# Performance work log

Measured on AMD Instinct MI355X. Metric: run time of the kernel, lower is better.

The kernel has to match this reference:

```python
import jax, jax.numpy as jnp
import numpy as np

D = 1024
H = 16
HD = D // H
DFF = 4 * D
LN_EPS = 1e-5

def layernorm(x, gamma, beta):
    mu = jnp.mean(x, axis=-1, keepdims=True)
    var = jnp.mean(jnp.square(x - mu), axis=-1, keepdims=True)
    return (x - mu) * jax.lax.rsqrt(var + LN_EPS) * gamma + beta

def setup_inputs() -> dict:
    key = jax.random.key(0)
    ks = jax.random.split(key, 10)
    B, Nq, Nk = 2, 2048, 2048
    s = 0.02
    return {
        "q_x": jax.random.normal(ks[0], (B, Nq, D), jnp.float32),
        "kv_x": jax.random.normal(ks[1], (B, Nk, D), jnp.float32),
        "Wq": jax.random.normal(ks[2], (D, D), jnp.float32) * s,
        "Wkv": jax.random.normal(ks[3], (2 * D, D), jnp.float32) * s,
        "Wo": jax.random.normal(ks[4], (D, D), jnp.float32) * s,
        "bo": jnp.zeros((D,), jnp.float32),
        "ln_q_g": jnp.ones((D,), jnp.float32),
        "ln_q_b": jnp.zeros((D,), jnp.float32),
        "ln_kv_g": jnp.ones((D,), jnp.float32),
        "ln_kv_b": jnp.zeros((D,), jnp.float32),
        "W1": jax.random.normal(ks[5], (DFF, D), jnp.float32) * s,
        "b1": jnp.zeros((DFF,), jnp.float32),
        "W2": jax.random.normal(ks[6], (D, DFF), jnp.float32) * s,
        "b2": jnp.zeros((D,), jnp.float32),
    }

def reference(q_x, kv_x, Wq, Wkv, Wo, bo, ln_q_g, ln_q_b, ln_kv_g, ln_kv_b, W1, b1, W2, b2):
    B, Nq, _ = q_x.shape
    Nk = kv_x.shape[1]
    scale = HD ** -0.5
    # norm + projections
    q = layernorm(q_x, ln_q_g, ln_q_b) @ Wq.T                    # [B,Nq,D]
    kv = layernorm(kv_x, ln_kv_g, ln_kv_b) @ Wkv.T               # [B,Nk,2D]
    q = q.reshape(B, Nq, H, HD).transpose(0, 2, 1, 3)            # [B,H,Nq,hd]
    kv = kv.reshape(B, Nk, 2, H, HD).transpose(2, 0, 3, 1, 4)    # [2,B,H,Nk,hd]
    k, v = kv[0], kv[1]
    attn = jnp.einsum('bhqd,bhkd->bhqk', q, k) * scale           # [B,H,Nq,Nk]
    attn = jax.nn.softmax(attn, axis=-1)
    out = jnp.einsum('bhqk,bhkd->bhqd', attn, v)
    out = out.transpose(0, 2, 1, 3).reshape(B, Nq, D)
    x = q_x + out @ Wo.T + bo
    h = jax.nn.silu(x @ W1.T + b1)
    x = x + h @ W2.T + b2
    return x
```

## Files before the change

### kernel.cpp

```cpp
#include <hip/hip_runtime.h>

using u16   = unsigned short;
using f32x4 = __attribute__((ext_vector_type(4))) float;
using s16x8 = __attribute__((ext_vector_type(8))) short;
using u32x2 = __attribute__((ext_vector_type(2))) unsigned int;
using u32x4 = __attribute__((ext_vector_type(4))) unsigned int;

#define LOG2E 1.44269504088896f

static __device__ __forceinline__ u16 f2bf(float f) {
  union { float f; unsigned u; } a; a.f = f;
  unsigned r = a.u + 0x7fffu + ((a.u >> 16) & 1u);
  return (u16)(r >> 16);
}
static __device__ __forceinline__ unsigned cvtpk(float lo, float hi) {
  unsigned r;
  asm("v_cvt_pk_bf16_f32 %0, %1, %2" : "=v"(r) : "v"(lo), "v"(hi));
  return r;
}

static __device__ __forceinline__ void gload16(const void* g, void* l) {
  __builtin_amdgcn_global_load_lds(
      (__attribute__((address_space(1))) unsigned int*)g,
      (__attribute__((address_space(3))) unsigned int*)l, 16, 0, 0);
}

static __device__ __forceinline__ int xcd_swz(int b, int nb) {
  return (b & 7) * (nb >> 3) + (b >> 3);
}

__global__ __launch_bounds__(256) void prep_k(
    const float* __restrict__ Wq, const float* __restrict__ Wkv,
    const float* __restrict__ Wo, const float* __restrict__ W1,
    const float* __restrict__ W2,
    u16* __restrict__ wq_b, u16* __restrict__ wkv_b, u16* __restrict__ wo_b,
    u16* __restrict__ w1_b, u16* __restrict__ w2_b,
    const float* __restrict__ xq, const float* __restrict__ xk,
    const float* __restrict__ gq, const float* __restrict__ bq,
    const float* __restrict__ gk, const float* __restrict__ bk,
    u16* __restrict__ oq, u16* __restrict__ ok)
{
  const int blk = blockIdx.x, t = threadIdx.x;
  if (blk < 12288) {
    const int i = blk * 256 + t;
    const float* src; u16* dst; int off; float sc = 1.0f;
    if      (i <  262144) { src = Wq;  dst = wq_b;  off = i; sc = 0.125f * LOG2E; }
    else if (i <  786432) { src = Wkv; dst = wkv_b; off = i -  262144; }
    else if (i < 1048576) { src = Wo;  dst = wo_b;  off = i -  786432; }
    else if (i < 2097152) { src = W1;  dst = w1_b;  off = i - 1048576; }
    else                  { src = W2;  dst = w2_b;  off = i - 2097152; }
    const float4 v = ((const float4*)src)[off];
    ushort4 o;
    o.x = f2bf(v.x * sc); o.y = f2bf(v.y * sc); o.z = f2bf(v.z * sc); o.w = f2bf(v.w * sc);
    ((ushort4*)dst)[off] = o;
    return;
  }
  int row = blk - 12288;
  const float* x; const float* gam; const float* bet; u16* out;
  if (row < 4096) { x = xq; gam = gq; bet = bq; out = oq; }
  else { row -= 4096; x = xk; gam = gk; bet = bk; out = ok; }
  const float4 v = ((const float4*)(x + (size_t)row * 1024))[t];
  float s  = v.x + v.y + v.z + v.w;
  float ss = v.x*v.x + v.y*v.y + v.z*v.z + v.w*v.w;
  #pragma unroll
  for (int m = 1; m < 64; m <<= 1) { s += __shfl_xor(s, m); ss += __shfl_xor(ss, m); }
  __shared__ float red[8];
  const int w = t >> 6;
  if ((t & 63) == 0) { red[w] = s; red[4 + w] = ss; }
  __syncthreads();
  s  = red[0] + red[1] + red[2] + red[3];
  ss = red[4] + red[5] + red[6] + red[7];
  const float mu   = s * (1.0f / 1024.0f);
  const float rstd = rsqrtf(ss * (1.0f / 1024.0f) - mu * mu + 1e-5f);
  const float4 gv = ((const float4*)gam)[t];
  const float4 bv = ((const float4*)bet)[t];
  ushort4 o;
  o.x = f2bf((v.x - mu) * rstd * gv.x + bv.x);
  o.y = f2bf((v.y - mu) * rstd * gv.y + bv.y);
  o.z = f2bf((v.z - mu) * rstd * gv.z + bv.z);
  o.w = f2bf((v.w - mu) * rstd * gv.w + bv.w);
  ((ushort4*)(out + (size_t)row * 1024))[t] = o;
}

template<int BIAS, int RES, int SILU, int OF32, int OBF>
static __device__ __forceinline__ void gemm_body64(
    const u16* __restrict__ A, const u16* __restrict__ B,
    u16* __restrict__ Cb, float* __restrict__ Cf,
    const float* __restrict__ bias, const float* __restrict__ resid,
    int N, int K, int bid, u16* smem)
{
  const int tid = threadIdx.x;
  const int w = tid >> 6, l = tid & 63;
  const int g = l >> 4, q = l & 15;
  const int ntn = N >> 6;
  const int bm = bid / ntn, bn = bid - bm * ntn;
  const int wr = w >> 1, wc = w & 1;
  const int sw = (q & 7) << 4;
  f32x4 acc[2][2] = {};

  const size_t abase = (size_t)(bm * 128) * K;
  const size_t bbase = (size_t)(bn * 64) * K;

  auto stage = [&](int buf, int k0) {
    u16* as = smem + buf * 8192;
    u16* bs = smem + 16384 + buf * 4096;
    #pragma unroll
    for (int r = 0; r < 2; ++r) {
      const int c = (r << 9) + tid;
      const int row = c >> 3;
      const int sp = (c & 7) ^ (row & 7);
      gload16(A + abase + (size_t)row * K + k0 + sp * 8,
              as + (size_t)((r << 9) + (w << 6)) * 8);
    }
    const int row = tid >> 3;
    const int sp = (tid & 7) ^ (row & 7);
    gload16(B + bbase + (size_t)row * K + k0 + sp * 8,
            bs + (size_t)(w << 6) * 8);
  };

  const int NT = K >> 6;
  stage(0, 0);
  asm volatile("s_waitcnt vmcnt(0)" ::: "memory");
  __syncthreads();
  int cur = 0;
  for (int t = 0; t < NT; ++t) {
    if (t + 1 < NT) stage(cur ^ 1, (t + 1) << 6);
    const char* as = (const char*)(smem + cur * 8192);
    const char* bs = (const char*)(smem + 16384 + cur * 4096);
    #pragma unroll
    for (int ks = 0; ks < 2; ++ks) {
      s16x8 af[2], bfr[2];
      #pragma unroll
      for (int m = 0; m < 2; ++m)
        af[m] = *(const s16x8*)(as + (size_t)(wr * 32 + m * 16 + q) * 128 +
                                ((ks * 64 + g * 16) ^ sw));
      #pragma unroll
      for (int n = 0; n < 2; ++n)
        bfr[n] = *(const s16x8*)(bs + (size_t)(wc * 32 + n * 16 + q) * 128 +
                                 ((ks * 64 + g * 16) ^ sw));
      #pragma unroll
      for (int m = 0; m < 2; ++m)
        #pragma unroll
        for (int n = 0; n < 2; ++n)
          acc[m][n] = __builtin_amdgcn_mfma_f32_16x16x32_bf16(af[m], bfr[n], acc[m][n], 0, 0, 0);
    }
    asm volatile("s_waitcnt vmcnt(0)" ::: "memory");
    __syncthreads();
    cur ^= 1;
  }

  #pragma unroll
  for (int m = 0; m < 2; ++m) {
    const int row0 = bm * 128 + wr * 32 + m * 16 + g * 4;
    #pragma unroll
    for (int n = 0; n < 2; ++n) {
      const int col = bn * 64 + wc * 32 + n * 16 + q;
      float bv = 0.0f;
      if (BIAS) bv = bias[col];
      #pragma unroll
      for (int r = 0; r < 4; ++r) {
        const size_t idx = (size_t)(row0 + r) * N + col;
        float v = acc[m][n][r] + bv;
        if (RES)  v += resid[idx];
        if (SILU) v = v / (1.0f + __expf(-v));
        if (OF32) Cf[idx] = v;
        if (OBF)  Cb[idx] = f2bf(v);
      }
    }
  }
}

template<int BIAS, int RES, int SILU, int OF32, int OBF>
__global__ __launch_bounds__(512, 4) void gemm_k(
    const u16* __restrict__ A, const u16* __restrict__ B,
    u16* __restrict__ Cb, float* __restrict__ Cf,
    const float* __restrict__ bias, const float* __restrict__ resid,
    int N, int K)
{
  __shared__ u16 smem[24576];
  const int bid = xcd_swz(blockIdx.x, gridDim.x);
  gemm_body64<BIAS, RES, SILU, OF32, OBF>(A, B, Cb, Cf, bias, resid, N, K, bid, smem);
}

__global__ __launch_bounds__(512, 4) void gemm_qkv_k(
    const u16* __restrict__ lnq, const u16* __restrict__ wq, u16* __restrict__ qp,
    const u16* __restrict__ lnk, const u16* __restrict__ wkv, u16* __restrict__ kvp)
{
  __shared__ u16 smem[24576];
  const int sbid = xcd_swz(blockIdx.x, 1536);
  if (sbid < 512)
    gemm_body64<0,0,0,0,1>(lnq, wq, qp, nullptr, nullptr, nullptr, 1024, 1024,
                           sbid, smem);
  else
    gemm_body64<0,0,0,0,1>(lnk, wkv, kvp, nullptr, nullptr, nullptr, 2048, 1024,
                           sbid - 512, smem);
}

template<int BIAS, int RES, int SILU, int OF32, int OBF>
__global__ __launch_bounds__(512, 2) void gemm256_k(
    const u16* __restrict__ A, const u16* __restrict__ B,
    u16* __restrict__ Cb, float* __restrict__ Cf,
    const float* __restrict__ bias, const float* __restrict__ resid,
    int N, int K)
{
  __shared__ u16 smem[65536];
  char* smem_c = (char*)smem;
  const int tid = threadIdx.x;
  const int w = tid >> 6, l = tid & 63;
  const int g = l >> 4, q = l & 15;
  const int wm = w >> 2, wn = w & 3;
  const int ntn = N >> 8;
  const int bid = xcd_swz(blockIdx.x, gridDim.x);
  const int bm = bid / ntn, bn = bid - bm * ntn;

  const size_t abase = (size_t)(bm * 256) * K;
  const size_t bbase = (size_t)(bn * 256) * K;

  f32x4 acc[8][4] = {};

  auto stage2 = [&](int buf, int kt, int part) {
    const int isB = part & 1, khalf = part >> 1;
    #pragma unroll
    for (int sub = 0; sub < 2; ++sub) {
      const int row  = sub * 128 + (tid >> 2);
      const int slot = (tid & 3) ^ ((row >> 1) & 3);
      const u16* src = (isB ? B + bbase : A + abase)
                     + (size_t)row * K + kt * 64 + khalf * 32 + slot * 8;
      char* dst = smem_c + buf * 65536 + isB * 32768 + khalf * 16384
                + sub * 8192 + w * 1024;
      gload16(src, dst);
    }
  };

  const int NT = K >> 6;
  stage2(0, 0, 0); stage2(0, 0, 1); stage2(0, 0, 2); stage2(0, 0, 3);
  int cur = 0;
  const int so = (g ^ ((q >> 1) & 3)) * 16;
  for (int t = 0; t < NT; ++t) {
    const bool pre = (t + 1 < NT);
    const char* base = smem_c + cur * 65536;
    #pragma unroll
    for (int ks = 0; ks < 2; ++ks) {
      if (ks == 0 || pre) asm volatile("s_waitcnt vmcnt(4)" ::: "memory");
      else                asm volatile("s_waitcnt vmcnt(0)" ::: "memory");
      asm volatile("" ::: "memory");
      __builtin_amdgcn_s_barrier();
      asm volatile("" ::: "memory");
      const char* Ab = base + ks * 16384;
      const char* Bb = base + 32768 + ks * 16384;
      s16x8 af[8], bf0[2];
      #pragma unroll
      for (int m = 0; m < 8; ++m)
        af[m] = *(const s16x8*)(Ab + (wm * 128 + m * 16 + q) * 64 + so);
      #pragma unroll
      for (int n = 0; n < 2; ++n)
        bf0[n] = *(const s16x8*)(Bb + (wn * 64 + n * 16 + q) * 64 + so);
      if (pre) stage2(cur ^ 1, t + 1, ks * 2);
      asm volatile("s_waitcnt lgkmcnt(0)" ::: "memory");
      __builtin_amdgcn_sched_barrier(0);
      __builtin_amdgcn_s_setprio(1);
      #pragma unroll
      for (int m = 0; m < 8; ++m) {
        acc[m][0] = __builtin_amdgcn_mfma_f32_16x16x32_bf16(af[m], bf0[0], acc[m][0], 0, 0, 0);
        acc[m][1] = __builtin_amdgcn_mfma_f32_16x16x32_bf16(af[m], bf0[1], acc[m][1], 0, 0, 0);
      }
      __builtin_amdgcn_s_setprio(0);
      s16x8 bf1[2];
      #pragma unroll
      for (int n = 0; n < 2; ++n)
        bf1[n] = *(const s16x8*)(Bb + (wn * 64 + (2 + n) * 16 + q) * 64 + so);
      if (pre) stage2(cur ^ 1, t + 1, ks * 2 + 1);
      asm volatile("s_waitcnt lgkmcnt(0)" ::: "memory");
      __builtin_amdgcn_sched_barrier(0);
      __builtin_amdgcn_s_setprio(1);
      #pragma unroll
      for (int m = 0; m < 8; ++m) {
        acc[m][2] = __builtin_amdgcn_mfma_f32_16x16x32_bf16(af[m], bf1[0], acc[m][2], 0, 0, 0);
        acc[m][3] = __builtin_amdgcn_mfma_f32_16x16x32_bf16(af[m], bf1[1], acc[m][3], 0, 0, 0);
      }
      __builtin_amdgcn_s_setprio(0);
    }
    cur ^= 1;
  }

  #pragma unroll
  for (int m = 0; m < 8; ++m) {
    const int row0 = bm * 256 + wm * 128 + m * 16 + g * 4;
    #pragma unroll
    for (int n = 0; n < 4; ++n) {
      const int col = bn * 256 + wn * 64 + n * 16 + q;
      float bv = 0.0f;
      if (BIAS) bv = bias[col];
      #pragma unroll
      for (int r = 0; r < 4; ++r) {
        const size_t idx = (size_t)(row0 + r) * N + col;
        float v = acc[m][n][r] + bv;
        if (RES)  v += resid[idx];
        if (SILU) v = v / (1.0f + __expf(-v));
        if (OF32) Cf[idx] = v;
        if (OBF)  Cb[idx] = f2bf(v);
      }
    }
  }
}

__global__ __launch_bounds__(256, 4) void attn_k(
    const u16* __restrict__ Q, const u16* __restrict__ KV, u16* __restrict__ O)
{
  __shared__ u16 Ks[2][64 * 64];
  __shared__ u16 Vs[2][64 * 64];
  const int tid = threadIdx.x;
  const int w = tid >> 6, l = tid & 63;
  const int g = l >> 4, q = l & 15;
  const int idx = blockIdx.x >> 3;
  const int bh = (blockIdx.x & 7) * 4 + (idx >> 5);
  const int qt = idx & 31;
  const int b = bh >> 4, h = bh & 15;

  const size_t qrow = (size_t)(b * 2048 + qt * 64 + w * 16 + q);
  s16x8 qf[2];
  qf[0] = *(const s16x8*)&Q[qrow * 1024 + h * 64 + g * 8];
  qf[1] = *(const s16x8*)&Q[qrow * 1024 + h * 64 + 32 + g * 8];

  f32x4 oacc[4] = {};
  float lrow = 0.0f;

  const u16* kvb = KV + (size_t)b * 2048 * 2048;
  const unsigned vs_base =
      (unsigned)(unsigned long long)(__attribute__((address_space(3))) u16*)Vs;

  auto stage = [&](int buf, int kv0) {
    #pragma unroll
    for (int r = 0; r < 2; ++r) {
      const int c = (r << 8) + tid;
      const int krow = c >> 3, slot = c & 7;
      gload16(kvb + (size_t)(kv0 + krow) * 2048 + h * 64 + ((slot ^ (krow & 7)) << 3),
              &Ks[buf][(size_t)((r << 8) + (w << 6)) * 8]);
      const int vkv = ((c >> 3) & 15) * 4 + ((c >> 1) & 3);
      const int vd0 = ((c >> 7) & 3) * 16 + (c & 1) * 8;
      gload16(kvb + (size_t)(kv0 + vkv) * 2048 + 1024 + h * 64 + vd0,
              &Vs[buf][(size_t)((r << 8) + (w << 6)) * 8]);
    }
  };

  stage(0, 0);
  asm volatile("s_waitcnt vmcnt(0)" ::: "memory");
  __syncthreads();
  int cur = 0;

  for (int kt = 0; kt < 32; ++kt) {
    if (kt + 1 < 32) stage(cur ^ 1, (kt + 1) * 64);

    const char* ksb = (const char*)Ks[cur];
    f32x4 sacc[4] = {};
    __builtin_amdgcn_s_setprio(1);
    #pragma unroll
    for (int s = 0; s < 2; ++s)
      #pragma unroll
      for (int nf = 0; nf < 4; ++nf) {
        const int krw = nf * 16 + q;
        const s16x8 kf = *(const s16x8*)(ksb + krw * 128 +
                              ((s * 64 + g * 16) ^ ((krw & 7) << 4)));
        sacc[nf] = __builtin_amdgcn_mfma_f32_16x16x32_bf16(kf, qf[s], sacc[nf], 0, 0, 0);
      }
    __builtin_amdgcn_s_setprio(0);

    #pragma unroll
    for (int nf = 0; nf < 4; ++nf)
      #pragma unroll
      for (int r = 0; r < 4; ++r)
        sacc[nf][r] = __builtin_amdgcn_exp2f(sacc[nf][r]);
    float rs0 = (sacc[0][0] + sacc[0][1]) + (sacc[0][2] + sacc[0][3]);
    float rs1 = (sacc[1][0] + sacc[1][1]) + (sacc[1][2] + sacc[1][3]);
    float rs2 = (sacc[2][0] + sacc[2][1]) + (sacc[2][2] + sacc[2][3]);
    float rs3 = (sacc[3][0] + sacc[3][1]) + (sacc[3][2] + sacc[3][3]);
    float rs = (rs0 + rs1) + (rs2 + rs3);
    rs += __shfl_xor(rs, 16);
    rs += __shfl_xor(rs, 32);
    lrow += rs;

    union { u32x4 u; s16x8 s8; } au[2];
    #pragma unroll
    for (int s = 0; s < 2; ++s) {
      au[s].u[0] = cvtpk(sacc[2*s  ][0], sacc[2*s  ][1]);
      au[s].u[1] = cvtpk(sacc[2*s  ][2], sacc[2*s  ][3]);
      au[s].u[2] = cvtpk(sacc[2*s+1][0], sacc[2*s+1][1]);
      au[s].u[3] = cvtpk(sacc[2*s+1][2], sacc[2*s+1][3]);
    }

    const unsigned a0 = vs_base + (unsigned)(cur << 13) + (unsigned)(g * 128 + 2 * q);
    u32x2 v0,v1,v2,v3,v4,v5,v6,v7,v8,v9,v10,v11,v12,v13,v14,v15;
    asm volatile(
        "ds_read_b64_tr_b16 %0,  %16\n\t"
        "ds_read_b64_tr_b16 %1,  %16 offset:512\n\t"
        "ds_read_b64_tr_b16 %2,  %16 offset:2048\n\t"
        "ds_read_b64_tr_b16 %3,  %16 offset:2560\n\t"
        "ds_read_b64_tr_b16 %4,  %16 offset:4096\n\t"
        "ds_read_b64_tr_b16 %5,  %16 offset:4608\n\t"
        "ds_read_b64_tr_b16 %6,  %16 offset:6144\n\t"
        "ds_read_b64_tr_b16 %7,  %16 offset:6656\n\t"
        "ds_read_b64_tr_b16 %8,  %16 offset:1024\n\t"
        "ds_read_b64_tr_b16 %9,  %16 offset:1536\n\t"
        "ds_read_b64_tr_b16 %10, %16 offset:3072\n\t"
        "ds_read_b64_tr_b16 %11, %16 offset:3584\n\t"
        "ds_read_b64_tr_b16 %12, %16 offset:5120\n\t"
        "ds_read_b64_tr_b16 %13, %16 offset:5632\n\t"
        "ds_read_b64_tr_b16 %14, %16 offset:7168\n\t"
        "ds_read_b64_tr_b16 %15, %16 offset:7680\n\t"
        "s_waitcnt lgkmcnt(0)"
        : "=&v"(v0), "=&v"(v1), "=&v"(v2),  "=&v"(v3),
          "=&v"(v4), "=&v"(v5), "=&v"(v6),  "=&v"(v7),
          "=&v"(v8), "=&v"(v9), "=&v"(v10), "=&v"(v11),
          "=&v"(v12),"=&v"(v13),"=&v"(v14), "=&v"(v15)
        : "v"(a0) : "memory");
    __builtin_amdgcn_sched_barrier(0);

    __builtin_amdgcn_s_setprio(1);
    {
      union { u32x4 u; s16x8 s8; } bu;
      bu.u[0]=v0[0];  bu.u[1]=v0[1];  bu.u[2]=v1[0];  bu.u[3]=v1[1];
      oacc[0] = __builtin_amdgcn_mfma_f32_16x16x32_bf16(au[0].s8, bu.s8, oacc[0], 0, 0, 0);
      bu.u[0]=v2[0];  bu.u[1]=v2[1];  bu.u[2]=v3[0];  bu.u[3]=v3[1];
      oacc[1] = __builtin_amdgcn_mfma_f32_16x16x32_bf16(au[0].s8, bu.s8, oacc[1], 0, 0, 0);
      bu.u[0]=v4[0];  bu.u[1]=v4[1];  bu.u[2]=v5[0];  bu.u[3]=v5[1];
      oacc[2] = __builtin_amdgcn_mfma_f32_16x16x32_bf16(au[0].s8, bu.s8, oacc[2], 0, 0, 0);
      bu.u[0]=v6[0];  bu.u[1]=v6[1];  bu.u[2]=v7[0];  bu.u[3]=v7[1];
      oacc[3] = __builtin_amdgcn_mfma_f32_16x16x32_bf16(au[0].s8, bu.s8, oacc[3], 0, 0, 0);
      bu.u[0]=v8[0];  bu.u[1]=v8[1];  bu.u[2]=v9[0];  bu.u[3]=v9[1];
      oacc[0] = __builtin_amdgcn_mfma_f32_16x16x32_bf16(au[1].s8, bu.s8, oacc[0], 0, 0, 0);
      bu.u[0]=v10[0]; bu.u[1]=v10[1]; bu.u[2]=v11[0]; bu.u[3]=v11[1];
      oacc[1] = __builtin_amdgcn_mfma_f32_16x16x32_bf16(au[1].s8, bu.s8, oacc[1], 0, 0, 0);
      bu.u[0]=v12[0]; bu.u[1]=v12[1]; bu.u[2]=v13[0]; bu.u[3]=v13[1];
      oacc[2] = __builtin_amdgcn_mfma_f32_16x16x32_bf16(au[1].s8, bu.s8, oacc[2], 0, 0, 0);
      bu.u[0]=v14[0]; bu.u[1]=v14[1]; bu.u[2]=v15[0]; bu.u[3]=v15[1];
      oacc[3] = __builtin_amdgcn_mfma_f32_16x16x32_bf16(au[1].s8, bu.s8, oacc[3], 0, 0, 0);
    }
    __builtin_amdgcn_s_setprio(0);

    asm volatile("s_waitcnt vmcnt(0)" ::: "memory");
    __syncthreads();
    cur ^= 1;
  }

  float lr[4];
  #pragma unroll
  for (int r = 0; r < 4; ++r) lr[r] = __shfl(lrow, g * 4 + r);
  const size_t ob = (size_t)(b * 2048 + qt * 64 + w * 16) * 1024 + h * 64;
  #pragma unroll
  for (int r = 0; r < 4; ++r) {
    const float inv = 1.0f / lr[r];
    #pragma unroll
    for (int nf = 0; nf < 4; ++nf)
      O[ob + (size_t)(g * 4 + r) * 1024 + nf * 16 + q] = f2bf(oacc[nf][r] * inv);
  }
}

extern "C" void kernel_launch(void* const* d_in, const int* in_sizes, int n_in,
                              void* d_out, int out_size, void* d_ws, size_t ws_size,
                              hipStream_t stream)
{
  const float* q_x  = (const float*)d_in[0];
  const float* kv_x = (const float*)d_in[1];
  const float* Wq   = (const float*)d_in[2];
  const float* Wkv  = (const float*)d_in[3];
  const float* Wo   = (const float*)d_in[4];
  const float* bo   = (const float*)d_in[5];
  const float* lnqg = (const float*)d_in[6];
  const float* lnqb = (const float*)d_in[7];
  const float* lnkg = (const float*)d_in[8];
  const float* lnkb = (const float*)d_in[9];
  const float* W1   = (const float*)d_in[10];
  const float* b1   = (const float*)d_in[11];
  const float* W2   = (const float*)d_in[12];
  const float* b2   = (const float*)d_in[13];
  float* out = (float*)d_out;

  char* ws = (char*)d_ws;
  const size_t MB = 1024 * 1024;
  u16*   wq_b  = (u16*)  (ws +  0 * MB);
  u16*   wkv_b = (u16*)  (ws +  2 * MB);
  u16*   wo_b  = (u16*)  (ws +  6 * MB);
  u16*   w1_b  = (u16*)  (ws +  8 * MB);
  u16*   w2_b  = (u16*)  (ws + 16 * MB);
  u16*   lnq   = (u16*)  (ws + 24 * MB);
  u16*   lnk   = (u16*)  (ws + 32 * MB);
  u16*   qp    = (u16*)  (ws + 40 * MB);
  u16*   kvp   = (u16*)  (ws + 48 * MB);
  u16*   ao    = (u16*)  (ws + 64 * MB);
  float* xf    = (float*)(ws + 72 * MB);
  u16*   xb    = (u16*)  (ws + 88 * MB);
  u16*   hb    = (u16*)  (ws + 96 * MB);

  prep_k<<<dim3(20480), dim3(256), 0, stream>>>(
      Wq, Wkv, Wo, W1, W2, wq_b, wkv_b, wo_b, w1_b, w2_b,
      q_x, kv_x, lnqg, lnqb, lnkg, lnkb, lnq, lnk);

  gemm_qkv_k<<<dim3(1536), dim3(512), 0, stream>>>(lnq, wq_b, qp, lnk, wkv_b, kvp);
  attn_k<<<dim3(1024), dim3(256), 0, stream>>>(qp, kvp, ao);
  gemm_k<1,1,0,1,1><<<dim3(512),  dim3(512), 0, stream>>>(
      ao, wo_b, xb, xf, bo, q_x, 1024, 1024);
  gemm256_k<1,0,1,0,1><<<dim3(256), dim3(512), 0, stream>>>(
      xb, w1_b, hb, nullptr, b1, nullptr, 4096, 1024);
  gemm_k<1,1,0,1,0><<<dim3(512),  dim3(512), 0, stream>>>(
      hb, w2_b, nullptr, out, b2, xf, 1024, 4096);
}
```

Measured before the change: 200.8 us.

## Triple-buffer attention K/V tiles with 512-thread blocks and deferred row sums

Attention blocks grow from 4 to 8 waves, so each block covers 128 query rows. This halves the grid and shares each staged K/V tile across twice as many queries. The K/V staging becomes a three-deep ring: a partial vmcnt wait plus one barrier per iteration lets the next tile's loads overlap compute, replacing the full drain and two-sync pattern. The per-iteration row-sum reduction with shuffles is replaced by a vector accumulator that is reduced once at the end. LDS use rises to 48KB per block, which may limit how many blocks fit on a CU.

After: 195.1 us. 2.8% less time.

```diff
diff --git a/kernel.cpp b/kernel.cpp
--- a/kernel.cpp
+++ b/kernel.cpp
@@ -304,52 +304,52 @@
   }
 }
 
-__global__ __launch_bounds__(256, 4) void attn_k(
+__global__ __launch_bounds__(512, 4) void attn_k(
     const u16* __restrict__ Q, const u16* __restrict__ KV, u16* __restrict__ O)
 {
-  __shared__ u16 Ks[2][64 * 64];
-  __shared__ u16 Vs[2][64 * 64];
+  __shared__ u16 Ks[3][64 * 64];
+  __shared__ u16 Vs[3][64 * 64];
   const int tid = threadIdx.x;
   const int w = tid >> 6, l = tid & 63;
   const int g = l >> 4, q = l & 15;
   const int idx = blockIdx.x >> 3;
-  const int bh = (blockIdx.x & 7) * 4 + (idx >> 5);
-  const int qt = idx & 31;
+  const int bh = (blockIdx.x & 7) * 4 + (idx >> 4);
+  const int qt = idx & 15;
   const int b = bh >> 4, h = bh & 15;
 
-  const size_t qrow = (size_t)(b * 2048 + qt * 64 + w * 16 + q);
+  const size_t qrow = (size_t)(b * 2048 + qt * 128 + w * 16 + q);
   s16x8 qf[2];
   qf[0] = *(const s16x8*)&Q[qrow * 1024 + h * 64 + g * 8];
   qf[1] = *(const s16x8*)&Q[qrow * 1024 + h * 64 + 32 + g * 8];
 
   f32x4 oacc[4] = {};
-  float lrow = 0.0f;
+  f32x4 ls = {0.0f, 0.0f, 0.0f, 0.0f};
 
   const u16* kvb = KV + (size_t)b * 2048 * 2048;
   const unsigned vs_base =
       (unsigned)(unsigned long long)(__attribute__((address_space(3))) u16*)Vs;
 
   auto stage = [&](int buf, int kv0) {
-    #pragma unroll
-    for (int r = 0; r < 2; ++r) {
-      const int c = (r << 8) + tid;
-      const int krow = c >> 3, slot = c & 7;
-      gload16(kvb + (size_t)(kv0 + krow) * 2048 + h * 64 + ((slot ^ (krow & 7)) << 3),
-              &Ks[buf][(size_t)((r << 8) + (w << 6)) * 8]);
-      const int vkv = ((c >> 3) & 15) * 4 + ((c >> 1) & 3);
-      const int vd0 = ((c >> 7) & 3) * 16 + (c & 1) * 8;
-      gload16(kvb + (size_t)(kv0 + vkv) * 2048 + 1024 + h * 64 + vd0,
-              &Vs[buf][(size_t)((r << 8) + (w << 6)) * 8]);
-    }
+    const int c = tid;
+    const int krow = c >> 3, slot = c & 7;
+    gload16(kvb + (size_t)(kv0 + krow) * 2048 + h * 64 + ((slot ^ (krow & 7)) << 3),
+            &Ks[buf][(size_t)(w << 6) * 8]);
+    const int vkv = ((c >> 3) & 15) * 4 + ((c >> 1) & 3);
+    const int vd0 = ((c >> 7) & 3) * 16 + (c & 1) * 8;
+    gload16(kvb + (size_t)(kv0 + vkv) * 2048 + 1024 + h * 64 + vd0,
+            &Vs[buf][(size_t)(w << 6) * 8]);
   };
 
   stage(0, 0);
-  asm volatile("s_waitcnt vmcnt(0)" ::: "memory");
-  __syncthreads();
+  stage(1, 64);
   int cur = 0;
 
   for (int kt = 0; kt < 32; ++kt) {
-    if (kt + 1 < 32) stage(cur ^ 1, (kt + 1) * 64);
+    if (kt < 31) asm volatile("s_waitcnt vmcnt(2)" ::: "memory");
+    else         asm volatile("s_waitcnt vmcnt(0)" ::: "memory");
+    __builtin_amdgcn_s_barrier();
+    asm volatile("" ::: "memory");
+    if (kt + 2 < 32) stage((cur == 0) ? 2 : cur - 1, (kt + 2) * 64);
 
     const char* ksb = (const char*)Ks[cur];
     f32x4 sacc[4] = {};
@@ -370,14 +370,7 @@
       #pragma unroll
       for (int r = 0; r < 4; ++r)
         sacc[nf][r] = __builtin_amdgcn_exp2f(sacc[nf][r]);
-    float rs0 = (sacc[0][0] + sacc[0][1]) + (sacc[0][2] + sacc[0][3]);
-    float rs1 = (sacc[1][0] + sacc[1][1]) + (sacc[1][2] + sacc[1][3]);
-    float rs2 = (sacc[2][0] + sacc[2][1]) + (sacc[2][2] + sacc[2][3]);
-    float rs3 = (sacc[3][0] + sacc[3][1]) + (sacc[3][2] + sacc[3][3]);
-    float rs = (rs0 + rs1) + (rs2 + rs3);
-    rs += __shfl_xor(rs, 16);
-    rs += __shfl_xor(rs, 32);
-    lrow += rs;
+    ls += sacc[0]; ls += sacc[1]; ls += sacc[2]; ls += sacc[3];
 
     union { u32x4 u; s16x8 s8; } au[2];
     #pragma unroll
@@ -388,7 +381,7 @@
       au[s].u[3] = cvtpk(sacc[2*s+1][2], sacc[2*s+1][3]);
     }
 
-    const unsigned a0 = vs_base + (unsigned)(cur << 13) + (unsigned)(g * 128 + 2 * q);
+    const unsigned a0 = vs_base + (unsigned)(cur * 8192) + (unsigned)(g * 128 + 2 * q);
     u32x2 v0,v1,v2,v3,v4,v5,v6,v7,v8,v9,v10,v11,v12,v13,v14,v15;
     asm volatile(
         "ds_read_b64_tr_b16 %0,  %16\n\t"
@@ -437,15 +430,16 @@
     }
     __builtin_amdgcn_s_setprio(0);
 
-    asm volatile("s_waitcnt vmcnt(0)" ::: "memory");
-    __syncthreads();
-    cur ^= 1;
-  }
-
+    cur = (cur == 2) ? 0 : cur + 1;
+  }
+
+  float lsum = (ls[0] + ls[1]) + (ls[2] + ls[3]);
+  lsum += __shfl_xor(lsum, 16);
+  lsum += __shfl_xor(lsum, 32);
   float lr[4];
   #pragma unroll
-  for (int r = 0; r < 4; ++r) lr[r] = __shfl(lrow, g * 4 + r);
-  const size_t ob = (size_t)(b * 2048 + qt * 64 + w * 16) * 1024 + h * 64;
+  for (int r = 0; r < 4; ++r) lr[r] = __shfl(lsum, g * 4 + r);
+  const size_t ob = (size_t)(b * 2048 + qt * 128 + w * 16) * 1024 + h * 64;
   #pragma unroll
   for (int r = 0; r < 4; ++r) {
     const float inv = 1.0f / lr[r];
@@ -496,7 +490,7 @@
       q_x, kv_x, lnqg, lnqb, lnkg, lnkb, lnq, lnk);
 
   gemm_qkv_k<<<dim3(1536), dim3(512), 0, stream>>>(lnq, wq_b, qp, lnk, wkv_b, kvp);
-  attn_k<<<dim3(1024), dim3(256), 0, stream>>>(qp, kvp, ao);
+  attn_k<<<dim3(512), dim3(512), 0, stream>>>(qp, kvp, ao);
   gemm_k<1,1,0,1,1><<<dim3(512),  dim3(512), 0, stream>>>(
       ao, wo_b, xb, xf, bo, q_x, 1024, 1024);
   gemm256_k<1,0,1,0,1><<<dim3(256), dim3(512), 0, stream>>>(
```
